# Kernel optimization log

Hardware: AMD Instinct MI355X
Metric: run time of the kernel (lower is better)

## Reference

```python
import jax, jax.numpy as jnp
import numpy as np

B_SZ, H_DIM, W_DIM, D_MODEL = 2, 64, 64, 192
N_STATE = 16   # d_state
R_RANK = 12    # dt_rank
K_DIRS = 4
LN_EPS = 1e-5


def setup_inputs() -> dict:
    key = jax.random.key(0)
    ks = jax.random.split(key, 5)
    x = jax.random.normal(ks[0], (B_SZ, H_DIM, W_DIM, D_MODEL), jnp.float32)
    # x_proj Linear weights, small init so dt/B/C projections stay numerically tame
    x_proj_weight = jax.random.normal(ks[1], (K_DIRS, R_RANK + 2 * N_STATE, D_MODEL), jnp.float32) * 0.02
    # dt_proj weight ~ U(-rank^-0.5, rank^-0.5) as in dt_init('random')
    dt_projs_weight = jax.random.uniform(ks[2], (K_DIRS, D_MODEL, R_RANK), jnp.float32,
                                         -(R_RANK ** -0.5), R_RANK ** -0.5)
    # dt bias = inverse-softplus of dt sampled log-uniform in [1e-3, 0.1]
    dt = jnp.exp(jax.random.uniform(ks[3], (K_DIRS, D_MODEL)) * (np.log(0.1) - np.log(1e-3)) + np.log(1e-3))
    dt = jnp.clip(dt, 1e-4, None)
    dt_projs_bias = dt + jnp.log(-jnp.expm1(-dt))
    # A_log_init: log(arange(1..N)) tiled over K*D rows
    A_logs = jnp.log(jnp.tile(jnp.arange(1, N_STATE + 1, dtype=jnp.float32), (K_DIRS * D_MODEL, 1)))
    Ds = jnp.ones((K_DIRS * D_MODEL,), jnp.float32)
    ln_weight = jnp.ones((D_MODEL,), jnp.float32)
    ln_bias = jnp.zeros((D_MODEL,), jnp.float32)
    return dict(x=x, x_proj_weight=x_proj_weight, dt_projs_weight=dt_projs_weight,
                dt_projs_bias=dt_projs_bias, A_logs=A_logs, Ds=Ds,
                ln_weight=ln_weight, ln_bias=ln_bias)


def _cross_scan(x):  # x: (B, D, H, W) -> (B, 4, D, L)
    b, d, h, w = x.shape
    x0 = x.reshape(b, d, h * w)                                  # row-major scan
    x1 = jnp.transpose(x, (0, 1, 3, 2)).reshape(b, d, h * w)     # column-major scan
    xs = jnp.stack([x0, x1], axis=1)
    return jnp.concatenate([xs, jnp.flip(xs, axis=-1)], axis=1)  # + both reversed


def _cross_merge(ys, h, w):  # ys: (B, 4, D, L) -> (B, D, L)
    b, _, d, l = ys.shape
    ys = ys[:, 0:2] + jnp.flip(ys[:, 2:4], axis=-1)
    y1 = jnp.transpose(ys[:, 1].reshape(b, d, w, h), (0, 1, 3, 2)).reshape(b, d, l)
    return ys[:, 0] + y1


def _selective_scan(xs, dts, A, Bs, Cs):
    # xs, dts: (B, K, D, L); A: (K, D, N); Bs, Cs: (B, K, N, L). dts already softplus'd.
    b, k, d, l = xs.shape
    n = A.shape[-1]

    @jax.checkpoint
    def step(h_prev, t):
        x_t, dt_t, B_t, C_t = t                         # (B,K,D),(B,K,D),(B,K,N),(B,K,N)
        dA = jnp.exp(dt_t[..., None] * A)               # (B,K,D,N)
        dBx = (dt_t * x_t)[..., None] * B_t[:, :, None, :]
        h = dA * h_prev + dBx
        y = jnp.einsum('bkdn,bkn->bkd', h, C_t)
        return h, y

    seq = (jnp.moveaxis(xs, -1, 0), jnp.moveaxis(dts, -1, 0),
           jnp.moveaxis(Bs, -1, 0), jnp.moveaxis(Cs, -1, 0))
    h0 = jnp.zeros((b, k, d, n), xs.dtype)
    _, ys = jax.lax.scan(step, h0, seq)                 # ys: (L,B,K,D)
    return jnp.moveaxis(ys, 0, -1)                      # (B,K,D,L)


def reference(x, x_proj_weight, dt_projs_weight, dt_projs_bias, A_logs, Ds, ln_weight, ln_bias):
    b, h, w, d = x.shape
    l = h * w
    xc = jnp.transpose(x, (0, 3, 1, 2))                  # (B, D, H, W)
    xs = _cross_scan(xc)                                 # (B, K, D, L)
    x_dbl = jnp.einsum('bkdl,kcd->bkcl', xs, x_proj_weight)
    dts, Bs, Cs = jnp.split(x_dbl, [R_RANK, R_RANK + N_STATE], axis=2)
    dts = jnp.einsum('bkrl,kdr->bkdl', dts, dt_projs_weight)
    dts = jax.nn.softplus(dts + dt_projs_bias[None, :, :, None])   # delta_softplus + bias
    A = -jnp.exp(A_logs).reshape(K_DIRS, d, N_STATE)
    ys = _selective_scan(xs, dts, A, Bs, Cs)             # (B, K, D, L)
    ys = ys + Ds.reshape(1, K_DIRS, d, 1) * xs           # D skip connection
    y = _cross_merge(ys, h, w)                           # (B, D, L)
    y = jnp.transpose(y, (0, 2, 1))                      # (B, L, D)
    mu = jnp.mean(y, -1, keepdims=True)
    var = jnp.mean(jnp.square(y - mu), -1, keepdims=True)
    y = (y - mu) * jax.lax.rsqrt(var + LN_EPS) * ln_weight + ln_bias   # out_norm LayerNorm
    return y.reshape(b, h, w, d)
```

## Files before the change

### kernel.cpp

```cpp
#include <hip/hip_runtime.h>
#include <math.h>

#define B_SZ 2
#define HH 64
#define WW 64
#define DM 192
#define NS 16
#define RR 12
#define KD 4
#define LL (HH * WW)
#define CPROJ (RR + 2 * NS)
#define CPAD 48
#define SCH 16
#define TLP 64
#define LOG2E 1.44269504088896340736f

__device__ __forceinline__ int spatial_idx(int k, int t) {
    if (k == 0) return t;
    if (k == 1) return ((t & 63) << 6) | (t >> 6);
    if (k == 2) return LL - 1 - t;
    int tp = LL - 1 - t;
    return ((tp & 63) << 6) | (tp >> 6);
}

__global__ __launch_bounds__(256) void proj_kernel(const float* __restrict__ x,
                                                   const float* __restrict__ xpw,
                                                   float* __restrict__ xdbl) {
    int blk = blockIdx.x;
    int ltile = blk % (LL / TLP);
    int bk = blk / (LL / TLP);
    int k = bk & 3;
    int b = bk >> 2;
    int l0 = ltile * TLP;

    __shared__ float xt[DM * (TLP + 1)];

    {
        int li = threadIdx.x >> 2;
        int d0 = (threadIdx.x & 3) * 48;
        int s = spatial_idx(k, l0 + li);
        const float4* xr = (const float4*)(x + ((size_t)b * LL + s) * DM + d0);
#pragma unroll
        for (int q = 0; q < 12; ++q) {
            float4 v = xr[q];
            int d = d0 + q * 4;
            xt[(d + 0) * (TLP + 1) + li] = v.x;
            xt[(d + 1) * (TLP + 1) + li] = v.y;
            xt[(d + 2) * (TLP + 1) + li] = v.z;
            xt[(d + 3) * (TLP + 1) + li] = v.w;
        }
    }
    __syncthreads();

    int lane = threadIdx.x & 63;
    int wv = threadIdx.x >> 6;
    int c0 = __builtin_amdgcn_readfirstlane(wv * 11);
    const float* wk = xpw + (size_t)k * CPROJ * DM;

    float acc[11];
#pragma unroll
    for (int ci = 0; ci < 11; ++ci) acc[ci] = 0.f;

    for (int d = 0; d < DM; ++d) {
        float xv = xt[d * (TLP + 1) + lane];
#pragma unroll
        for (int ci = 0; ci < 11; ++ci)
            acc[ci] = fmaf(xv, wk[(size_t)(c0 + ci) * DM + d], acc[ci]);
    }
    float* orow = xdbl + ((size_t)bk * LL + l0 + lane) * CPAD;
#pragma unroll
    for (int ci = 0; ci < 11; ++ci) orow[c0 + ci] = acc[ci];
}

template <int PHASE, int NCHT>
__global__ __launch_bounds__(192) void scan_kernel(
    const float* __restrict__ x, const float* __restrict__ xdbl,
    const float* __restrict__ dtw, const float* __restrict__ dtb,
    const float* __restrict__ Alogs, const float* __restrict__ Ds,
    float* __restrict__ carry, float* __restrict__ aprod, float* __restrict__ ybuf) {
    const int CHT = LL / NCHT;
    int blk = blockIdx.x;
    int chunk = blk % NCHT;
    int bk = blk / NCHT;
    int k = bk & 3;
    int b = bk >> 2;
    int d = threadIdx.x;
    int kd = k * DM + d;

    float Wdt[RR];
#pragma unroll
    for (int r = 0; r < RR; ++r) Wdt[r] = dtw[(size_t)kd * RR + r];
    float bias = dtb[kd];
    float Avl2[NS];
#pragma unroll
    for (int n = 0; n < NS; ++n) Avl2[n] = -__expf(Alogs[(size_t)kd * NS + n]) * LOG2E;
    float Dval = Ds[kd];

    bool pws = true;
#pragma unroll
    for (int n = 0; n < NS; ++n)
        pws = pws && (fabsf(Avl2[n] - (float)(n + 1) * Avl2[0]) <= 1e-5f * fabsf(Avl2[n]) + 1e-30f);
    const bool pw = (__all(pws ? 1 : 0) != 0);

    float h[NS];
    float dtsum = 0.f;
    size_t cbase = ((size_t)(bk * NCHT + chunk) * DM + d) * NS;
    if (PHASE == 1) {
#pragma unroll
        for (int n = 0; n < NS; ++n) h[n] = 0.f;
    } else {
#pragma unroll
        for (int n = 0; n < NS; ++n) h[n] = carry[cbase + n];
    }

    __shared__ float lds[SCH * CPAD];
    int tbase = chunk * CHT;
    for (int t0 = tbase; t0 < tbase + CHT; t0 += SCH) {
        __syncthreads();
        for (int i = threadIdx.x; i < SCH * CPAD; i += DM)
            lds[i] = xdbl[((size_t)bk * LL + t0) * CPAD + i];
        __syncthreads();
        for (int tt = 0; tt < SCH; ++tt) {
            const float* row = lds + tt * CPAD;
            int t = t0 + tt;
            float z = bias;
#pragma unroll
            for (int r = 0; r < RR; ++r) z = fmaf(row[r], Wdt[r], z);
            float dt = (z > 15.f) ? z : __logf(1.f + __expf(z));
            int s = spatial_idx(k, t);
            float xv = x[((size_t)b * LL + s) * DM + d];
            float dtx = dt * xv;

            float dA[NS];
            if (pw) {
                float e1 = exp2f(dt * Avl2[0]);
                dA[0] = e1;
                dA[1] = e1 * e1;
                dA[2] = dA[1] * e1;
                dA[3] = dA[1] * dA[1];
                dA[4] = dA[3] * e1;
                dA[5] = dA[3] * dA[1];
                dA[6] = dA[3] * dA[2];
                dA[7] = dA[3] * dA[3];
                dA[8] = dA[7] * e1;
                dA[9] = dA[7] * dA[1];
                dA[10] = dA[7] * dA[2];
                dA[11] = dA[7] * dA[3];
                dA[12] = dA[7] * dA[4];
                dA[13] = dA[7] * dA[5];
                dA[14] = dA[7] * dA[6];
                dA[15] = dA[7] * dA[7];
            } else {
#pragma unroll
                for (int n = 0; n < NS; ++n) dA[n] = exp2f(dt * Avl2[n]);
            }

            float y = 0.f;
#pragma unroll
            for (int n = 0; n < NS; ++n) {
                h[n] = fmaf(dA[n], h[n], dtx * row[RR + n]);
                if (PHASE == 3) y = fmaf(h[n], row[RR + NS + n], y);
            }
            if (PHASE == 1) dtsum += dt;
            if (PHASE == 3) {
                atomicAdd(&ybuf[((size_t)b * LL + s) * DM + d], y + Dval * xv);
            }
        }
    }
    if (PHASE == 1) {
#pragma unroll
        for (int n = 0; n < NS; ++n) {
            carry[cbase + n] = h[n];
            aprod[cbase + n] = exp2f(dtsum * Avl2[n]);
        }
    }
}

template <int NCHT>
__global__ __launch_bounds__(256) void fix_kernel(float* __restrict__ carry,
                                                  const float* __restrict__ aprod) {
    int idx = blockIdx.x * 256 + threadIdx.x;
    int n = idx & (NS - 1);
    int dn = idx >> 4;
    int d = dn % DM;
    int bk = dn / DM;
    size_t base = ((size_t)bk * NCHT * DM + d) * NS + n;
    const size_t stride = (size_t)DM * NS;
    float hp = 0.f;
    for (int c = 0; c < NCHT; ++c) {
        size_t off = base + (size_t)c * stride;
        float P = aprod[off];
        float Cr = carry[off];
        carry[off] = hp;
        hp = fmaf(P, hp, Cr);
    }
}

__global__ __launch_bounds__(256) void ln_kernel(const float* __restrict__ ybuf,
                                                 const float* __restrict__ lnw,
                                                 const float* __restrict__ lnb,
                                                 float* __restrict__ out) {
    int row = blockIdx.x * 4 + (threadIdx.x >> 6);
    int lane = threadIdx.x & 63;
    const float* yr = ybuf + (size_t)row * DM;
    float v0 = yr[lane], v1 = yr[lane + 64], v2 = yr[lane + 128];
    float s = v0 + v1 + v2;
    float sq = v0 * v0 + v1 * v1 + v2 * v2;
#pragma unroll
    for (int off = 32; off >= 1; off >>= 1) {
        s += __shfl_xor(s, off, 64);
        sq += __shfl_xor(sq, off, 64);
    }
    float mu = s * (1.f / DM);
    float var = sq * (1.f / DM) - mu * mu;
    float inv = rsqrtf(var + 1e-5f);
    float* orow = out + (size_t)row * DM;
    orow[lane]       = (v0 - mu) * inv * lnw[lane]       + lnb[lane];
    orow[lane + 64]  = (v1 - mu) * inv * lnw[lane + 64]  + lnb[lane + 64];
    orow[lane + 128] = (v2 - mu) * inv * lnw[lane + 128] + lnb[lane + 128];
}

extern "C" void kernel_launch(void* const* d_in, const int* in_sizes, int n_in,
                              void* d_out, int out_size, void* d_ws, size_t ws_size,
                              hipStream_t stream) {
    const float* x    = (const float*)d_in[0];
    const float* xpw  = (const float*)d_in[1];
    const float* dtw  = (const float*)d_in[2];
    const float* dtb  = (const float*)d_in[3];
    const float* Alog = (const float*)d_in[4];
    const float* Ds   = (const float*)d_in[5];
    const float* lnw  = (const float*)d_in[6];
    const float* lnb  = (const float*)d_in[7];
    float* out = (float*)d_out;

    const size_t F_XD   = (size_t)B_SZ * KD * LL * CPAD;
    const size_t F_C64  = (size_t)B_SZ * KD * 64 * DM * NS;
    const size_t F_C128 = 2 * F_C64;
    const size_t F_YB   = (size_t)B_SZ * LL * DM;

    float* ws   = (float*)d_ws;
    float* xdbl = ws;

    proj_kernel<<<B_SZ * KD * (LL / TLP), 256, 0, stream>>>(x, xpw, xdbl);

    if (ws_size >= (F_XD + 2 * F_C128) * sizeof(float)) {
        float* carry = xdbl + F_XD;
        float* aprod = carry + F_C128;
        float* ybuf  = aprod;
        scan_kernel<1, 128><<<B_SZ * KD * 128, DM, 0, stream>>>(x, xdbl, dtw, dtb, Alog, Ds,
                                                                carry, aprod, ybuf);
        fix_kernel<128><<<(B_SZ * KD * DM * NS) / 256, 256, 0, stream>>>(carry, aprod);
        hipMemsetAsync(ybuf, 0, F_YB * sizeof(float), stream);
        scan_kernel<3, 128><<<B_SZ * KD * 128, DM, 0, stream>>>(x, xdbl, dtw, dtb, Alog, Ds,
                                                                carry, aprod, ybuf);
        ln_kernel<<<(B_SZ * LL) / 4, 256, 0, stream>>>(ybuf, lnw, lnb, out);
    } else {
        float* carry = xdbl + F_XD;
        float* aprod = carry + F_C64;
        float* ybuf  = aprod + F_C64;
        scan_kernel<1, 64><<<B_SZ * KD * 64, DM, 0, stream>>>(x, xdbl, dtw, dtb, Alog, Ds,
                                                              carry, aprod, ybuf);
        fix_kernel<64><<<(B_SZ * KD * DM * NS) / 256, 256, 0, stream>>>(carry, aprod);
        hipMemsetAsync(ybuf, 0, F_YB * sizeof(float), stream);
        scan_kernel<3, 64><<<B_SZ * KD * 64, DM, 0, stream>>>(x, xdbl, dtw, dtb, Alog, Ds,
                                                              carry, aprod, ybuf);
        ln_kernel<<<(B_SZ * LL) / 4, 256, 0, stream>>>(ybuf, lnw, lnb, out);
    }
}
```

Baseline: 100.9 us.

## Replace atomic output accumulation with per-direction buffers summed in layernorm

When the workspace is large enough, each scan direction writes its output into its own buffer with plain stores, and the layernorm kernel sums the four buffers before normalising. This removes the float atomics on the shared output and the memset that cleared it beforehand. The cost is four times the output memory, plus extra reads in the layernorm pass. The fallback path replaces hipMemsetAsync with a custom zero kernel and drops the 64-chunk variant. Softplus is also rewritten in terms of exp2/log2.

Measured after the change: 94.45 us. 1.07x faster.

```diff
diff --git a/kernel.cpp b/kernel.cpp
--- a/kernel.cpp
+++ b/kernel.cpp
@@ -14,6 +14,7 @@
 #define SCH 16
 #define TLP 64
 #define LOG2E 1.44269504088896340736f
+#define LN2F 0.69314718055994530942f
 
 __device__ __forceinline__ int spatial_idx(int k, int t) {
     if (k == 0) return t;
@@ -72,7 +73,7 @@
     for (int ci = 0; ci < 11; ++ci) orow[c0 + ci] = acc[ci];
 }
 
-template <int PHASE, int NCHT>
+template <int PHASE, int NCHT, int ATOMIC>
 __global__ __launch_bounds__(192) void scan_kernel(
     const float* __restrict__ x, const float* __restrict__ xdbl,
     const float* __restrict__ dtw, const float* __restrict__ dtb,
@@ -126,7 +127,7 @@
             float z = bias;
 #pragma unroll
             for (int r = 0; r < RR; ++r) z = fmaf(row[r], Wdt[r], z);
-            float dt = (z > 15.f) ? z : __logf(1.f + __expf(z));
+            float dt = (z > 15.f) ? z : __log2f(1.f + exp2f(z * LOG2E)) * LN2F;
             int s = spatial_idx(k, t);
             float xv = x[((size_t)b * LL + s) * DM + d];
             float dtx = dt * xv;
@@ -163,7 +164,10 @@
             }
             if (PHASE == 1) dtsum += dt;
             if (PHASE == 3) {
-                atomicAdd(&ybuf[((size_t)b * LL + s) * DM + d], y + Dval * xv);
+                float val = y + Dval * xv;
+                size_t oidx = ((size_t)b * LL + s) * DM + d;
+                if (ATOMIC) atomicAdd(&ybuf[oidx], val);
+                else        ybuf[(size_t)k * (B_SZ * LL * DM) + oidx] = val;
             }
         }
     }
@@ -196,14 +200,23 @@
     }
 }
 
+template <int NB>
 __global__ __launch_bounds__(256) void ln_kernel(const float* __restrict__ ybuf,
                                                  const float* __restrict__ lnw,
                                                  const float* __restrict__ lnb,
                                                  float* __restrict__ out) {
+    const size_t SEG = (size_t)B_SZ * LL * DM;
     int row = blockIdx.x * 4 + (threadIdx.x >> 6);
     int lane = threadIdx.x & 63;
     const float* yr = ybuf + (size_t)row * DM;
-    float v0 = yr[lane], v1 = yr[lane + 64], v2 = yr[lane + 128];
+    float v0 = 0.f, v1 = 0.f, v2 = 0.f;
+#pragma unroll
+    for (int kq = 0; kq < NB; ++kq) {
+        const float* p = yr + kq * SEG;
+        v0 += p[lane];
+        v1 += p[lane + 64];
+        v2 += p[lane + 128];
+    }
     float s = v0 + v1 + v2;
     float sq = v0 * v0 + v1 * v1 + v2 * v2;
 #pragma unroll
@@ -218,6 +231,11 @@
     orow[lane]       = (v0 - mu) * inv * lnw[lane]       + lnb[lane];
     orow[lane + 64]  = (v1 - mu) * inv * lnw[lane + 64]  + lnb[lane + 64];
     orow[lane + 128] = (v2 - mu) * inv * lnw[lane + 128] + lnb[lane + 128];
+}
+
+__global__ __launch_bounds__(256) void zero_kernel(float4* __restrict__ p, int n4) {
+    for (int i = blockIdx.x * 256 + threadIdx.x; i < n4; i += gridDim.x * 256)
+        p[i] = make_float4(0.f, 0.f, 0.f, 0.f);
 }
 
 extern "C" void kernel_launch(void* const* d_in, const int* in_sizes, int n_in,
@@ -243,27 +261,26 @@
 
     proj_kernel<<<B_SZ * KD * (LL / TLP), 256, 0, stream>>>(x, xpw, xdbl);
 
-    if (ws_size >= (F_XD + 2 * F_C128) * sizeof(float)) {
+    if (ws_size >= (F_XD + 2 * F_C128 + 4 * F_YB) * sizeof(float)) {
+        float* carry = xdbl + F_XD;
+        float* aprod = carry + F_C128;
+        float* ybuf4 = aprod + F_C128;
+        scan_kernel<1, 128, 0><<<B_SZ * KD * 128, DM, 0, stream>>>(x, xdbl, dtw, dtb, Alog, Ds,
+                                                                   carry, aprod, ybuf4);
+        fix_kernel<128><<<(B_SZ * KD * DM * NS) / 256, 256, 0, stream>>>(carry, aprod);
+        scan_kernel<3, 128, 0><<<B_SZ * KD * 128, DM, 0, stream>>>(x, xdbl, dtw, dtb, Alog, Ds,
+                                                                   carry, aprod, ybuf4);
+        ln_kernel<4><<<(B_SZ * LL) / 4, 256, 0, stream>>>(ybuf4, lnw, lnb, out);
+    } else {
         float* carry = xdbl + F_XD;
         float* aprod = carry + F_C128;
         float* ybuf  = aprod;
-        scan_kernel<1, 128><<<B_SZ * KD * 128, DM, 0, stream>>>(x, xdbl, dtw, dtb, Alog, Ds,
-                                                                carry, aprod, ybuf);
+        scan_kernel<1, 128, 1><<<B_SZ * KD * 128, DM, 0, stream>>>(x, xdbl, dtw, dtb, Alog, Ds,
+                                                                   carry, aprod, ybuf);
         fix_kernel<128><<<(B_SZ * KD * DM * NS) / 256, 256, 0, stream>>>(carry, aprod);
-        hipMemsetAsync(ybuf, 0, F_YB * sizeof(float), stream);
-        scan_kernel<3, 128><<<B_SZ * KD * 128, DM, 0, stream>>>(x, xdbl, dtw, dtb, Alog, Ds,
-                                                                carry, aprod, ybuf);
-        ln_kernel<<<(B_SZ * LL) / 4, 256, 0, stream>>>(ybuf, lnw, lnb, out);
-    } else {
-        float* carry = xdbl + F_XD;
-        float* aprod = carry + F_C64;
-        float* ybuf  = aprod + F_C64;
-        scan_kernel<1, 64><<<B_SZ * KD * 64, DM, 0, stream>>>(x, xdbl, dtw, dtb, Alog, Ds,
-                                                              carry, aprod, ybuf);
-        fix_kernel<64><<<(B_SZ * KD * DM * NS) / 256, 256, 0, stream>>>(carry, aprod);
-        hipMemsetAsync(ybuf, 0, F_YB * sizeof(float), stream);
-        scan_kernel<3, 64><<<B_SZ * KD * 64, DM, 0, stream>>>(x, xdbl, dtw, dtb, Alog, Ds,
-                                                              carry, aprod, ybuf);
-        ln_kernel<<<(B_SZ * LL) / 4, 256, 0, stream>>>(ybuf, lnw, lnb, out);
-    }
-}
+        zero_kernel<<<1024, 256, 0, stream>>>((float4*)ybuf, (int)(F_YB / 4));
+        scan_kernel<3, 128, 1><<<B_SZ * KD * 128, DM, 0, stream>>>(x, xdbl, dtw, dtb, Alog, Ds,
+                                                                   carry, aprod, ybuf);
+        ln_kernel<1><<<(B_SZ * LL) / 4, 256, 0, stream>>>(ybuf, lnw, lnb, out);
+    }
+}
```
